# Optimization experiments

Hardware: AMD Instinct MI355X
Metric: run time of the kernel (lower is better)

## Reference

```python
import jax, jax.numpy as jnp
import numpy as np

S_SIGMA = 8      # spatial downsampling of the bilateral grid
N_BINS = 16      # intensity bins (range resolution)
EPS = 1e-8


def _blur_axis(g, k, axis):
    """1D correlation of grid g with small tap filter k along `axis` (zero pad)."""
    taps = k.shape[0]
    r = taps // 2
    pad = [(0, 0)] * g.ndim
    pad[axis] = (r, r)
    gp = jnp.pad(g, pad)
    n = g.shape[axis]
    out = k[0] * jax.lax.slice_in_dim(gp, 0, n, axis=axis)
    for i in range(1, taps):
        out = out + k[i] * jax.lax.slice_in_dim(gp, i, i + n, axis=axis)
    return out


def _bilateral_one(img, fs, fr):
    """Bilateral grid splat -> blur -> slice for a single [H,W] channel.
    Guide signal is the channel itself (values assumed in [0,1])."""
    H, W = img.shape
    GH = (H - 1) // S_SIGMA + 2
    GW = (W - 1) // S_SIGMA + 2
    GZ = N_BINS + 1

    ys = jnp.arange(H, dtype=img.dtype)
    xs = jnp.arange(W, dtype=img.dtype)

    # ---- splat (nearest-cell scatter-add of homogeneous (value, weight)) ----
    gy = jnp.round(ys / S_SIGMA).astype(jnp.int32)            # [H]
    gx = jnp.round(xs / S_SIGMA).astype(jnp.int32)            # [W]
    gyg, gxg = jnp.meshgrid(gy, gx, indexing='ij')            # [H,W]
    gz = jnp.clip(jnp.round(img * (N_BINS - 1)), 0, N_BINS - 1).astype(jnp.int32)
    val = jnp.zeros((GH, GW, GZ), img.dtype).at[gyg, gxg, gz].add(img)
    wt = jnp.zeros((GH, GW, GZ), img.dtype).at[gyg, gxg, gz].add(jnp.ones_like(img))

    # ---- blur grid: learnable 5-tap filter_s along y,x and filter_r along z ----
    for axis, k in ((0, fs), (1, fs), (2, fr)):
        val = _blur_axis(val, k, axis)
        wt = _blur_axis(wt, k, axis)

    # ---- slice (trilinear gather at (y/s, x/s, I*(NB-1))) ----
    fy = ys / S_SIGMA
    fx = xs / S_SIGMA
    fz = jnp.clip(img * (N_BINS - 1), 0.0, N_BINS - 1)        # [H,W]
    y0 = jnp.floor(fy).astype(jnp.int32)
    x0 = jnp.floor(fx).astype(jnp.int32)
    z0 = jnp.floor(fz).astype(jnp.int32)
    y1 = jnp.minimum(y0 + 1, GH - 1)
    x1 = jnp.minimum(x0 + 1, GW - 1)
    z1 = jnp.minimum(z0 + 1, GZ - 1)
    ty = fy - y0.astype(img.dtype)                            # [H]
    tx = fx - x0.astype(img.dtype)                            # [W]
    tz = fz - z0.astype(img.dtype)                            # [H,W]

    out_v = jnp.zeros_like(img)
    out_w = jnp.zeros_like(img)
    for yi, wy in ((y0, 1.0 - ty), (y1, ty)):
        for xi, wx in ((x0, 1.0 - tx), (x1, tx)):
            for zi, wz in ((z0, 1.0 - tz), (z1, tz)):
                w = wy[:, None] * wx[None, :] * wz            # [H,W]
                out_v = out_v + w * val[yi[:, None], xi[None, :], zi]
                out_w = out_w + w * wt[yi[:, None], xi[None, :], zi]
    return out_v / (out_w + EPS)


def setup_inputs() -> dict:
    key = jax.random.key(0)
    k1, k2 = jax.random.split(key)
    blurred_batch = jax.random.uniform(k1, (4, 3, 1024, 1024), dtype=jnp.float32)
    kernel_batch = jax.random.uniform(k2, (4, 11, 11), dtype=jnp.float32)
    g = jnp.array([1.0, 4.0, 6.0, 4.0, 1.0], dtype=jnp.float32)
    g = g / g.sum()  # smooth 5-tap filter so the blur is nontrivial
    return {
        'blurred_batch': blurred_batch,
        'kernel_batch': kernel_batch,
        'filter_s': g,
        'filter_r': g,
        'num_irls_iter': 1,
        'num_cg_iter': 5,
    }


def reference(blurred_batch, kernel_batch, filter_s, filter_r, num_irls_iter, num_cg_iter):
    # kernel_batch, num_irls_iter, num_cg_iter are unused on this code path,
    # matching the original forward (only BilateralGrid.apply touches x).
    B, C, H, W = blurred_batch.shape
    imgs = blurred_batch.reshape(B * C, H, W)
    out = jax.vmap(lambda im: _bilateral_one(im, filter_s, filter_r))(imgs)
    return out.reshape(B, C, H, W)
```

## Files before the change

### kernel.cpp

```cpp
#include <hip/hip_runtime.h>

#define S_SIGMA 8
#define NBINS   16
#define HDIM    1024
#define WDIM    1024
#define GH      129
#define GW      129
#define GZ      17
#define CELLS   (GH*GW*GZ)
#define ROWSZ   (GW*GZ)
#define EPSV    1e-8f
#define FIXS    1048576.0f
#define FIXI    (1.0f/1048576.0f)

__global__ __launch_bounds__(64) void splat_gather_kernel(
    const float* __restrict__ img, float* __restrict__ grid, int nImg, int imgBase)
{
    __shared__ unsigned lval[16 * 64];
    __shared__ unsigned lwt [16 * 64];

    int tid = threadIdx.x;
    int idx = blockIdx.x * 64 + tid;
    int total = nImg * GH * GW;

    #pragma unroll
    for (int z = 0; z < 16; ++z) { lval[z * 64 + tid] = 0u; lwt[z * 64 + tid] = 0u; }

    if (idx < total) {
        int b   = idx / (GH * GW);
        int rem = idx - b * (GH * GW);
        int gy  = rem / GW;
        int gx  = rem - gy * GW;
        const float* ib = img + (size_t)(imgBase + b) * (HDIM * WDIM);

        bool interior = (gx >= 1) & (gx <= 127) & (gy >= 1) & (gy <= 127);
        if (interior) {
            int py = gy & 1, px = gx & 1;
            int ylo = 8 * gy - 4 + py;
            int nr  = 9 - 2 * py;
            int ax  = 8 * gx - 4;
            for (int r = 0; r < nr; ++r) {
                const float* rp = ib + (size_t)(ylo + r) * WDIM + ax;
                float4 A = *(const float4*)rp;
                float4 B = *(const float4*)(rp + 4);
                float  cv = rp[8];
                float e7[7] = {A.y, A.z, A.w, B.x, B.y, B.z, B.w};
                #pragma unroll
                for (int j = 0; j < 7; ++j) {
                    float v = e7[j];
                    int gz = min(max((int)rintf(v * 15.0f), 0), 15);
                    atomicAdd(&lval[gz * 64 + tid], (unsigned)rintf(v * FIXS));
                    atomicAdd(&lwt [gz * 64 + tid], 1u);
                }
                if (!px) {
                    int gz = min(max((int)rintf(A.x * 15.0f), 0), 15);
                    atomicAdd(&lval[gz * 64 + tid], (unsigned)rintf(A.x * FIXS));
                    atomicAdd(&lwt [gz * 64 + tid], 1u);
                    gz = min(max((int)rintf(cv * 15.0f), 0), 15);
                    atomicAdd(&lval[gz * 64 + tid], (unsigned)rintf(cv * FIXS));
                    atomicAdd(&lwt [gz * 64 + tid], 1u);
                }
            }
        } else {
            int ylo = max(0, 8 * gy - 4 + (gy & 1));
            int yhi = min(HDIM - 1, 8 * gy + 4 - (gy & 1));
            int xlo = max(0, 8 * gx - 4 + (gx & 1));
            int xhi = min(WDIM - 1, 8 * gx + 4 - (gx & 1));
            for (int y = ylo; y <= yhi; ++y) {
                const float* row = ib + (size_t)y * WDIM;
                for (int x = xlo; x <= xhi; ++x) {
                    float v = row[x];
                    int gz = min(max((int)rintf(v * 15.0f), 0), 15);
                    atomicAdd(&lval[gz * 64 + tid], (unsigned)rintf(v * FIXS));
                    atomicAdd(&lwt [gz * 64 + tid], 1u);
                }
            }
        }

        float2* dst = (float2*)grid + (size_t)idx * GZ;
        #pragma unroll
        for (int z = 0; z < 16; ++z) {
            float2 o;
            o.x = (float)lval[z * 64 + tid] * FIXI;
            o.y = (float)lwt [z * 64 + tid];
            dst[z] = o;
        }
        float2 zero; zero.x = 0.f; zero.y = 0.f;
        dst[16] = zero;
    }
}

#define TO 12
#define TI 16
#define NIN  (TI*TI*GZ)
#define NTMP (TO*TI*GZ)
#define NOUT (TO*TO*GZ)

__global__ __launch_bounds__(256) void blur_fused_kernel(
    const float2* __restrict__ in, float2* __restrict__ out,
    const float* __restrict__ kfs, const float* __restrict__ kfr)
{
    __shared__ float2 sbin[NIN];
    __shared__ float2 stmp[NTMP];

    int tid = threadIdx.x;
    int tx0 = blockIdx.x * TO;
    int ty0 = blockIdx.y * TO;
    int b   = blockIdx.z;

    float ks[5] = {kfs[0], kfs[1], kfs[2], kfs[3], kfs[4]};
    float kr[5] = {kfr[0], kfr[1], kfr[2], kfr[3], kfr[4]};

    const float2* gb = in + (size_t)b * CELLS;
    for (int li = tid; li < NIN; li += 256) {
        int iy = li / (TI * GZ);
        int r  = li - iy * (TI * GZ);
        int ix = r / GZ;
        int z  = r - ix * GZ;
        int gy = ty0 - 2 + iy;
        int gx = tx0 - 2 + ix;
        float2 v; v.x = 0.f; v.y = 0.f;
        if (gy >= 0 && gy < GH && gx >= 0 && gx < GW)
            v = gb[((size_t)gy * GW + gx) * GZ + z];
        sbin[li] = v;
    }
    __syncthreads();

    for (int o = tid; o < NTMP; o += 256) {
        int oy = o / (TI * GZ);
        int r  = o - oy * (TI * GZ);
        float2 a; a.x = 0.f; a.y = 0.f;
        #pragma unroll
        for (int t = 0; t < 5; ++t) {
            float2 g = sbin[(oy + t) * (TI * GZ) + r];
            a.x += ks[t] * g.x;
            a.y += ks[t] * g.y;
        }
        stmp[o] = a;
    }
    __syncthreads();

    for (int o = tid; o < NOUT; o += 256) {
        int oy = o / (TO * GZ);
        int r  = o - oy * (TO * GZ);
        int ox = r / GZ;
        int z  = r - ox * GZ;
        float2 a; a.x = 0.f; a.y = 0.f;
        #pragma unroll
        for (int t = 0; t < 5; ++t) {
            float2 g = stmp[(oy * TI + ox + t) * GZ + z];
            a.x += ks[t] * g.x;
            a.y += ks[t] * g.y;
        }
        sbin[o] = a;
    }
    __syncthreads();

    float2* ob = out + (size_t)b * CELLS;
    for (int o = tid; o < NOUT; o += 256) {
        int oy = o / (GZ * TO);
        int r2 = o - oy * (GZ * TO);
        int z  = r2 / TO;
        int ox = r2 - z * TO;
        int gy = ty0 + oy;
        int gx = tx0 + ox;
        if (gy < GH && gx < GW) {
            int cb = (oy * TO + ox) * GZ;
            float2 a; a.x = 0.f; a.y = 0.f;
            #pragma unroll
            for (int t = 0; t < 5; ++t) {
                int zz = z + t - 2;
                if (zz >= 0 && zz < GZ) {
                    float2 g = sbin[cb + zz];
                    a.x += kr[t] * g.x;
                    a.y += kr[t] * g.y;
                }
            }
            ob[((size_t)gy * GZ + z) * GW + gx] = a;
        }
    }
}

#define XP2   136
#define RST   XP2
#define ZST   (2*XP2)

__global__ __launch_bounds__(256) void slice_rows_kernel(
    const float* __restrict__ img, const float2* __restrict__ grid,
    float* __restrict__ out, int imgBase)
{
    __shared__ float2 sg[GZ * ZST];

    int tid = threadIdx.x;
    int k   = blockIdx.x;
    int b   = blockIdx.y;

    const float2* gsrc = grid + (size_t)b * CELLS + (size_t)k * ROWSZ;
    for (int i = tid; i < 2 * ROWSZ; i += 256) {
        int r   = i / ROWSZ;
        int rem = i - r * ROWSZ;
        int z   = rem / GW;
        int x0  = rem - z * GW;
        sg[z * ZST + r * RST + x0] = gsrc[i];
    }
    __syncthreads();

    int x   = tid << 2;
    int x0v = tid >> 1;
    float txb = (float)(x & 7) * 0.125f;

    size_t rowBase = (size_t)(imgBase + b) * (HDIM * WDIM) + (size_t)(k << 3) * WDIM + x;

    #pragma unroll
    for (int r = 0; r < 8; ++r) {
        size_t pixBase = rowBase + (size_t)r * WDIM;
        float4 v4 = *(const float4*)(img + pixBase);
        float ty = (float)r * 0.125f;
        float wy0 = 1.f - ty, wy1 = ty;

        float vv[4] = {v4.x, v4.y, v4.z, v4.w};
        float rr[4];
        #pragma unroll
        for (int j = 0; j < 4; ++j) {
            float v  = vv[j];
            float fz = fminf(fmaxf(v * 15.0f, 0.0f), 15.0f);
            float zf = floorf(fz);
            int   z0 = (int)zf;
            float tz = fz - zf;
            float tx = txb + (float)j * 0.125f;
            float wx0 = 1.f - tx, wx1 = tx;
            float wz0 = 1.f - tz, wz1 = tz;

            int base = z0 * ZST + x0v;
            float2 g000 = sg[base];
            float2 g010 = sg[base + 1];
            float2 g100 = sg[base + RST];
            float2 g110 = sg[base + RST + 1];
            float2 g001 = sg[base + ZST];
            float2 g011 = sg[base + ZST + 1];
            float2 g101 = sg[base + ZST + RST];
            float2 g111 = sg[base + ZST + RST + 1];

            float ov = 0.f, ow = 0.f, w;
            w = wy0 * wx0 * wz0; ov += w * g000.x; ow += w * g000.y;
            w = wy0 * wx0 * wz1; ov += w * g001.x; ow += w * g001.y;
            w = wy0 * wx1 * wz0; ov += w * g010.x; ow += w * g010.y;
            w = wy0 * wx1 * wz1; ov += w * g011.x; ow += w * g011.y;
            w = wy1 * wx0 * wz0; ov += w * g100.x; ow += w * g100.y;
            w = wy1 * wx0 * wz1; ov += w * g101.x; ow += w * g101.y;
            w = wy1 * wx1 * wz0; ov += w * g110.x; ow += w * g110.y;
            w = wy1 * wx1 * wz1; ov += w * g111.x; ow += w * g111.y;
            rr[j] = ov / (ow + EPSV);
        }
        float4 r4; r4.x = rr[0]; r4.y = rr[1]; r4.z = rr[2]; r4.w = rr[3];
        *(float4*)(out + pixBase) = r4;
    }
}

extern "C" void kernel_launch(void* const* d_in, const int* in_sizes, int n_in,
                              void* d_out, int out_size, void* d_ws, size_t ws_size,
                              hipStream_t stream)
{
    const float* img = (const float*)d_in[0];
    const float* fs  = (const float*)d_in[2];
    const float* fr  = (const float*)d_in[3];
    float* out = (float*)d_out;

    int nImgTotal = in_sizes[0] / (HDIM * WDIM);
    size_t perImgBytes = (size_t)CELLS * 2 * sizeof(float);

    int maxChunk = (int)(ws_size / (2 * perImgBytes));
    if (maxChunk < 1) return;
    if (maxChunk > nImgTotal) maxChunk = nImgTotal;

    const int tilesPerDim = (GH + TO - 1) / TO;

    for (int base = 0; base < nImgTotal; base += maxChunk) {
        int c = nImgTotal - base;
        if (c > maxChunk) c = maxChunk;

        float* A = (float*)d_ws;
        float* B = A + (size_t)c * CELLS * 2;

        int nCells = c * GH * GW;
        int colBlocks = (nCells + 63) / 64;
        splat_gather_kernel<<<colBlocks, 64, 0, stream>>>(img, A, c, base);

        dim3 bgrid(tilesPerDim, tilesPerDim, c);
        blur_fused_kernel<<<bgrid, 256, 0, stream>>>((const float2*)A, (float2*)B, fs, fr);

        dim3 sgrid(HDIM / 8, c);
        slice_rows_kernel<<<sgrid, 256, 0, stream>>>(img, (const float2*)B, out, base);
    }
}
```

Baseline: 106.2 us.

## Split splat rows across four waves per cell and drop blur temp buffer

The splat kernel now uses 256 threads per 64 grid cells. Each of four waves handles every fourth source row and accumulates into shared LDS histograms with atomics, and the writeback of the z bins is split across the waves. The blur kernel keeps its y- and x-pass intermediates in registers and writes them back into the single shared buffer after a barrier, which removes the separate stmp array and halves LDS use to allow more resident blocks. In exchange, the four waves now contend on the same LDS atomics, more barriers are added, and register pressure in the blur kernel goes up.

```diff
diff --git a/kernel.cpp b/kernel.cpp
--- a/kernel.cpp
+++ b/kernel.cpp
@@ -13,22 +13,24 @@
 #define FIXS    1048576.0f
 #define FIXI    (1.0f/1048576.0f)
 
-__global__ __launch_bounds__(64) void splat_gather_kernel(
+__global__ __launch_bounds__(256) void splat_gather_kernel(
     const float* __restrict__ img, float* __restrict__ grid, int nImg, int imgBase)
 {
     __shared__ unsigned lval[16 * 64];
     __shared__ unsigned lwt [16 * 64];
 
     int tid = threadIdx.x;
-    int idx = blockIdx.x * 64 + tid;
+    int c   = tid & 63;
+    int q   = tid >> 6;
+    int cellIdx = blockIdx.x * 64 + c;
     int total = nImg * GH * GW;
 
-    #pragma unroll
-    for (int z = 0; z < 16; ++z) { lval[z * 64 + tid] = 0u; lwt[z * 64 + tid] = 0u; }
-
-    if (idx < total) {
-        int b   = idx / (GH * GW);
-        int rem = idx - b * (GH * GW);
+    for (int i = tid; i < 16 * 64; i += 256) { lval[i] = 0u; lwt[i] = 0u; }
+    __syncthreads();
+
+    if (cellIdx < total) {
+        int b   = cellIdx / (GH * GW);
+        int rem = cellIdx - b * (GH * GW);
         int gy  = rem / GW;
         int gx  = rem - gy * GW;
         const float* ib = img + (size_t)(imgBase + b) * (HDIM * WDIM);
@@ -39,7 +41,7 @@
             int ylo = 8 * gy - 4 + py;
             int nr  = 9 - 2 * py;
             int ax  = 8 * gx - 4;
-            for (int r = 0; r < nr; ++r) {
+            for (int r = q; r < nr; r += 4) {
                 const float* rp = ib + (size_t)(ylo + r) * WDIM + ax;
                 float4 A = *(const float4*)rp;
                 float4 B = *(const float4*)(rp + 4);
@@ -49,16 +51,16 @@
                 for (int j = 0; j < 7; ++j) {
                     float v = e7[j];
                     int gz = min(max((int)rintf(v * 15.0f), 0), 15);
-                    atomicAdd(&lval[gz * 64 + tid], (unsigned)rintf(v * FIXS));
-                    atomicAdd(&lwt [gz * 64 + tid], 1u);
+                    atomicAdd(&lval[gz * 64 + c], (unsigned)rintf(v * FIXS));
+                    atomicAdd(&lwt [gz * 64 + c], 1u);
                 }
                 if (!px) {
                     int gz = min(max((int)rintf(A.x * 15.0f), 0), 15);
-                    atomicAdd(&lval[gz * 64 + tid], (unsigned)rintf(A.x * FIXS));
-                    atomicAdd(&lwt [gz * 64 + tid], 1u);
+                    atomicAdd(&lval[gz * 64 + c], (unsigned)rintf(A.x * FIXS));
+                    atomicAdd(&lwt [gz * 64 + c], 1u);
                     gz = min(max((int)rintf(cv * 15.0f), 0), 15);
-                    atomicAdd(&lval[gz * 64 + tid], (unsigned)rintf(cv * FIXS));
-                    atomicAdd(&lwt [gz * 64 + tid], 1u);
+                    atomicAdd(&lval[gz * 64 + c], (unsigned)rintf(cv * FIXS));
+                    atomicAdd(&lwt [gz * 64 + c], 1u);
                 }
             }
         } else {
@@ -66,27 +68,32 @@
             int yhi = min(HDIM - 1, 8 * gy + 4 - (gy & 1));
             int xlo = max(0, 8 * gx - 4 + (gx & 1));
             int xhi = min(WDIM - 1, 8 * gx + 4 - (gx & 1));
-            for (int y = ylo; y <= yhi; ++y) {
+            for (int y = ylo + q; y <= yhi; y += 4) {
                 const float* row = ib + (size_t)y * WDIM;
                 for (int x = xlo; x <= xhi; ++x) {
                     float v = row[x];
                     int gz = min(max((int)rintf(v * 15.0f), 0), 15);
-                    atomicAdd(&lval[gz * 64 + tid], (unsigned)rintf(v * FIXS));
-                    atomicAdd(&lwt [gz * 64 + tid], 1u);
+                    atomicAdd(&lval[gz * 64 + c], (unsigned)rintf(v * FIXS));
+                    atomicAdd(&lwt [gz * 64 + c], 1u);
                 }
             }
         }
-
-        float2* dst = (float2*)grid + (size_t)idx * GZ;
-        #pragma unroll
-        for (int z = 0; z < 16; ++z) {
+    }
+    __syncthreads();
+
+    if (cellIdx < total) {
+        float2* dst = (float2*)grid + (size_t)cellIdx * GZ;
+        int zlo = q * 4;
+        int zhi = (q == 3) ? 17 : zlo + 4;
+        for (int z = zlo; z < zhi; ++z) {
             float2 o;
-            o.x = (float)lval[z * 64 + tid] * FIXI;
-            o.y = (float)lwt [z * 64 + tid];
+            if (z == 16) { o.x = 0.f; o.y = 0.f; }
+            else {
+                o.x = (float)lval[z * 64 + c] * FIXI;
+                o.y = (float)lwt [z * 64 + c];
+            }
             dst[z] = o;
         }
-        float2 zero; zero.x = 0.f; zero.y = 0.f;
-        dst[16] = zero;
     }
 }
 
@@ -95,13 +102,14 @@
 #define NIN  (TI*TI*GZ)
 #define NTMP (TO*TI*GZ)
 #define NOUT (TO*TO*GZ)
+#define NTI  13
+#define NXI  10
 
 __global__ __launch_bounds__(256) void blur_fused_kernel(
     const float2* __restrict__ in, float2* __restrict__ out,
     const float* __restrict__ kfs, const float* __restrict__ kfr)
 {
     __shared__ float2 sbin[NIN];
-    __shared__ float2 stmp[NTMP];
 
     int tid = threadIdx.x;
     int tx0 = blockIdx.x * TO;
@@ -126,33 +134,55 @@
     }
     __syncthreads();
 
-    for (int o = tid; o < NTMP; o += 256) {
-        int oy = o / (TI * GZ);
-        int r  = o - oy * (TI * GZ);
+    float2 rt[NTI];
+    #pragma unroll
+    for (int it = 0; it < NTI; ++it) {
+        int o = tid + it * 256;
         float2 a; a.x = 0.f; a.y = 0.f;
-        #pragma unroll
-        for (int t = 0; t < 5; ++t) {
-            float2 g = sbin[(oy + t) * (TI * GZ) + r];
-            a.x += ks[t] * g.x;
-            a.y += ks[t] * g.y;
-        }
-        stmp[o] = a;
-    }
-    __syncthreads();
-
-    for (int o = tid; o < NOUT; o += 256) {
-        int oy = o / (TO * GZ);
-        int r  = o - oy * (TO * GZ);
-        int ox = r / GZ;
-        int z  = r - ox * GZ;
+        if (o < NTMP) {
+            int oy = o / (TI * GZ);
+            int r  = o - oy * (TI * GZ);
+            #pragma unroll
+            for (int t = 0; t < 5; ++t) {
+                float2 g = sbin[(oy + t) * (TI * GZ) + r];
+                a.x += ks[t] * g.x;
+                a.y += ks[t] * g.y;
+            }
+        }
+        rt[it] = a;
+    }
+    __syncthreads();
+    #pragma unroll
+    for (int it = 0; it < NTI; ++it) {
+        int o = tid + it * 256;
+        if (o < NTMP) sbin[o] = rt[it];
+    }
+    __syncthreads();
+
+    float2 rx[NXI];
+    #pragma unroll
+    for (int it = 0; it < NXI; ++it) {
+        int o = tid + it * 256;
         float2 a; a.x = 0.f; a.y = 0.f;
-        #pragma unroll
-        for (int t = 0; t < 5; ++t) {
-            float2 g = stmp[(oy * TI + ox + t) * GZ + z];
-            a.x += ks[t] * g.x;
-            a.y += ks[t] * g.y;
-        }
-        sbin[o] = a;
+        if (o < NOUT) {
+            int oy = o / (TO * GZ);
+            int r  = o - oy * (TO * GZ);
+            int ox = r / GZ;
+            int z  = r - ox * GZ;
+            #pragma unroll
+            for (int t = 0; t < 5; ++t) {
+                float2 g = sbin[(oy * TI + ox + t) * GZ + z];
+                a.x += ks[t] * g.x;
+                a.y += ks[t] * g.y;
+            }
+        }
+        rx[it] = a;
+    }
+    __syncthreads();
+    #pragma unroll
+    for (int it = 0; it < NXI; ++it) {
+        int o = tid + it * 256;
+        if (o < NOUT) sbin[o] = rx[it];
     }
     __syncthreads();
 
@@ -283,8 +313,8 @@
         float* B = A + (size_t)c * CELLS * 2;
 
         int nCells = c * GH * GW;
-        int colBlocks = (nCells + 63) / 64;
-        splat_gather_kernel<<<colBlocks, 64, 0, stream>>>(img, A, c, base);
+        int cellBlocks = (nCells + 63) / 64;
+        splat_gather_kernel<<<cellBlocks, 256, 0, stream>>>(img, A, c, base);
 
         dim3 bgrid(tilesPerDim, tilesPerDim, c);
         blur_fused_kernel<<<bgrid, 256, 0, stream>>>((const float2*)A, (float2*)B, fs, fr);
```

Result: faster. 93.43 us (-12.0%).
